# Performance work log

Measured on AMD Instinct MI355X. Metric: run time of the kernel, lower is better.

## Reference

```python
import jax, jax.numpy as jnp
import numpy as np

B, S, DIN, DOUT = 4, 2048, 4096, 4096

def setup_inputs() -> dict:
    key = jax.random.key(0)
    k1, k2, k3, k4 = jax.random.split(key, 4)
    x = jax.random.normal(k1, (B, S, DIN), dtype=jnp.float32)
    # int8-valued weights stored in int32 (harness dtype constraint); values in [-127, 127]
    weight_int8 = jax.random.randint(k2, (DOUT, DIN), -127, 128, dtype=jnp.int32)
    # per-output-channel scales, small positive values typical of int8 quantization
    scale = jax.random.uniform(k3, (DOUT,), dtype=jnp.float32, minval=1e-4, maxval=2e-2)
    bias = jax.random.normal(k4, (DOUT,), dtype=jnp.float32)
    return {"x": x, "weight_int8": weight_int8, "scale": scale, "bias": bias}

def reference(x, weight_int8, scale, bias):
    # Dequantize: w[o, i] = int8[o, i] * scale[o], cast to activation dtype
    w = (weight_int8.astype(jnp.float32) * scale[:, None]).astype(x.dtype)  # [DOUT, DIN]
    # F.linear: y = x @ w.T + bias
    return jnp.einsum('bsi,oi->bso', x, w) + bias
```

## Files before the change

### kernel.cpp

```cpp
#include <hip/hip_runtime.h>
#include <hip/hip_bf16.h>

#define BM 256
#define BN 256
#define BK 64
#define NSLOT 4
#define LDS_BYTES (2 * NSLOT * BM * BK)

typedef float  f32x4  __attribute__((ext_vector_type(4)));
typedef int    i32x4  __attribute__((ext_vector_type(4)));
typedef __bf16 bf16x8 __attribute__((ext_vector_type(8)));
typedef __bf16 bf16x4 __attribute__((ext_vector_type(4)));

__device__ __forceinline__ void gload_lds16(const void* g, void* l) {
    __builtin_amdgcn_global_load_lds(
        (const __attribute__((address_space(1))) void*)g,
        (__attribute__((address_space(3))) void*)l, 16, 0, 0);
}

__global__ __launch_bounds__(256)
void prep_fused(const float* __restrict__ x, const int* __restrict__ w,
                signed char* __restrict__ xq, unsigned* __restrict__ wq,
                float* __restrict__ xs, int K, int M, int n4w, int WB) {
    const int tid = threadIdx.x;
    const int b = blockIdx.x;

    if (b < M) {
        const float* xr = x + (size_t)b * K;
        const int n4 = K / 4;

        float mx = 0.f;
        for (int i = tid; i < n4; i += 256) {
            f32x4 v = ((const f32x4*)xr)[i];
            mx = fmaxf(mx, fmaxf(fmaxf(fabsf(v[0]), fabsf(v[1])),
                                 fmaxf(fabsf(v[2]), fabsf(v[3]))));
        }
#pragma unroll
        for (int off = 32; off; off >>= 1)
            mx = fmaxf(mx, __shfl_xor(mx, off));
        __shared__ float smx[4];
        if ((tid & 63) == 0) smx[tid >> 6] = mx;
        __syncthreads();
        mx = fmaxf(fmaxf(smx[0], smx[1]), fmaxf(smx[2], smx[3]));

        const float inv = mx > 0.f ? 127.f / mx : 0.f;
        if (tid == 0) xs[b] = mx / 127.f;

        unsigned* out = (unsigned*)(xq + (size_t)b * K);
        for (int i = tid; i < n4; i += 256) {
            f32x4 v = ((const f32x4*)xr)[i];
            int q0 = __float2int_rn(v[0] * inv);
            int q1 = __float2int_rn(v[1] * inv);
            int q2 = __float2int_rn(v[2] * inv);
            int q3 = __float2int_rn(v[3] * inv);
            out[i] = (unsigned)(q0 & 255) | ((unsigned)(q1 & 255) << 8) |
                     ((unsigned)(q2 & 255) << 16) | ((unsigned)(q3 & 255) << 24);
        }
    } else {
        int i = (b - M) * 256 + tid;
        const int stride = WB * 256;
        for (; i < n4w; i += stride) {
            i32x4 v = ((const i32x4*)w)[i];
            wq[i] = (unsigned)(v[0] & 255) | ((unsigned)(v[1] & 255) << 8) |
                    ((unsigned)(v[2] & 255) << 16) | ((unsigned)(v[3] & 255) << 24);
        }
    }
}


__global__ __launch_bounds__(512, 2)
void qlin_gemm_i8(const signed char* __restrict__ A,
                  const signed char* __restrict__ B,
                  const float* __restrict__ xs,
                  const float* __restrict__ scale,
                  const float* __restrict__ bias,
                  float* __restrict__ C, int M, int N, int K) {
    extern __shared__ signed char lds[];
    signed char* lA = lds;
    signed char* lB = lds + NSLOT * (BM * BK);

    const int NTN = N / BN;
    const int nwg = gridDim.x;
    int bid = blockIdx.x;
    bid = (bid & 7) * (nwg >> 3) + (bid >> 3);
    const int tm = bid / NTN;
    const int tn = bid % NTN;

    const int tid  = threadIdx.x;
    const int lane = tid & 63;
    const int wid  = tid >> 6;
    const int wr   = wid >> 2;
    const int wc   = wid & 3;

    const int srow0 = wid * 32 + (lane >> 2);
    const int srow1 = srow0 + 16;
    const int gq0 = (lane & 3) ^ ((srow0 >> 1) & 3);
    const int gq1 = (lane & 3) ^ ((srow1 >> 1) & 3);
    const signed char* Ap0 = A + (size_t)(tm * BM + srow0) * K + gq0 * 16;
    const signed char* Ap1 = A + (size_t)(tm * BM + srow1) * K + gq1 * 16;
    const signed char* Bp0 = B + (size_t)(tn * BN + srow0) * K + gq0 * 16;
    const signed char* Bp1 = B + (size_t)(tn * BN + srow1) * K + gq1 * 16;

    const int NT = K / BK;

    auto STAGE_A = [&](int t) {
        signed char* d = lA + (t & (NSLOT - 1)) * (BM * BK) + wid * 2048;
        gload_lds16(Ap0 + t * BK, d);
        gload_lds16(Ap1 + t * BK, d + 1024);
    };
    auto STAGE_B = [&](int t) {
        signed char* d = lB + (t & (NSLOT - 1)) * (BM * BK) + wid * 2048;
        gload_lds16(Bp0 + t * BK, d);
        gload_lds16(Bp1 + t * BK, d + 1024);
    };

    const int fr = lane & 15;
    const int kq = lane >> 4;

    auto AOFF = [&](int mi) {
        const int R = wr * 128 + mi * 16 + fr;
        return R * 64 + ((kq ^ ((R >> 1) & 3)) << 4);
    };
    auto BOFF = [&](int ni) {
        const int R = wc * 64 + ni * 16 + fr;
        return R * 64 + ((kq ^ ((R >> 1) & 3)) << 4);
    };

    i32x4 acc[8][4];
#pragma unroll
    for (int mi = 0; mi < 8; ++mi)
#pragma unroll
        for (int ni = 0; ni < 4; ++ni) {
            acc[mi][ni][0] = 0; acc[mi][ni][1] = 0;
            acc[mi][ni][2] = 0; acc[mi][ni][3] = 0;
        }

    for (int u = 0; u < 3 && u < NT; ++u) { STAGE_A(u); STAGE_B(u); }

    for (int t = 0; t < NT; ++t) {
        const signed char* lAs = lA + (t & (NSLOT - 1)) * (BM * BK);
        const signed char* lBs = lB + (t & (NSLOT - 1)) * (BM * BK);
        const int rem = NT - 1 - t;

        if (rem >= 2)      asm volatile("s_waitcnt vmcnt(8)" ::: "memory");
        else if (rem == 1) asm volatile("s_waitcnt vmcnt(4)" ::: "memory");
        else               asm volatile("s_waitcnt vmcnt(0)" ::: "memory");
        __builtin_amdgcn_s_barrier();

        i32x4 af[8], bf[4];
#pragma unroll
        for (int mi = 0; mi < 8; ++mi)
            af[mi] = *(const i32x4*)(lAs + AOFF(mi));
#pragma unroll
        for (int ni = 0; ni < 4; ++ni)
            bf[ni] = *(const i32x4*)(lBs + BOFF(ni));

        if (t + 3 < NT) { STAGE_A(t + 3); STAGE_B(t + 3); }

#pragma unroll
        for (int mi = 0; mi < 8; ++mi)
#pragma unroll
            for (int ni = 0; ni < 4; ++ni)
                acc[mi][ni] = __builtin_amdgcn_mfma_i32_16x16x64_i8(
                    af[mi], bf[ni], acc[mi][ni], 0, 0, 0);
    }

    const int rb = tm * BM + wr * 128 + (lane >> 4) * 4;
    const int cb = tn * BN + wc * 64 + fr;
#pragma unroll
    for (int mi = 0; mi < 8; ++mi) {
        const int m0 = rb + mi * 16;
        float sm[4];
#pragma unroll
        for (int r = 0; r < 4; ++r) sm[r] = xs[m0 + r];
#pragma unroll
        for (int ni = 0; ni < 4; ++ni) {
            const int n = cb + ni * 16;
            const float sc = scale[n];
            const float bs = bias[n];
#pragma unroll
            for (int r = 0; r < 4; ++r)
                C[(size_t)(m0 + r) * N + n] =
                    fmaf((float)acc[mi][ni][r], sm[r] * sc, bs);
        }
    }
}

#define FBM 128
#define FBK 32

__device__ __forceinline__ int swz_elem(int row, int e) {
    return row * FBK + (e ^ (((row >> 1) & 3) << 3));
}

__global__ __launch_bounds__(256, 2)
void qlin_gemm_reg(const float* __restrict__ A, const int* __restrict__ W,
                   const float* __restrict__ scale, const float* __restrict__ bias,
                   float* __restrict__ C, int M, int N, int K) {
    __shared__ __bf16 lA[2][FBM * FBK];
    __shared__ __bf16 lB[2][FBM * FBK];
    const int NTN = N / FBM;
    const int nwg = gridDim.x;
    int bid = blockIdx.x;
    if ((nwg & 7) == 0) bid = (bid & 7) * (nwg >> 3) + (bid >> 3);
    const int tm = bid / NTN, tn = bid % NTN;
    const int tid = threadIdx.x, lane = tid & 63, wid = tid >> 6;
    const int wr = wid >> 1, wc = wid & 1;
    const int srow0 = tid >> 3, skq = tid & 7;
    const float* aptr = A + (size_t)(tm * FBM + srow0) * K + skq * 4;
    const int*   wptr = W + (size_t)(tn * FBM + srow0) * K + skq * 4;
    const size_t rstride = (size_t)32 * K;
    f32x4 sa[4]; i32x4 sw[4];
    auto LOAD = [&](int t) {
#pragma unroll
        for (int j = 0; j < 4; ++j) {
            sa[j] = *(const f32x4*)(aptr + (size_t)t * FBK + j * rstride);
            sw[j] = *(const i32x4*)(wptr + (size_t)t * FBK + j * rstride);
        }
    };
    auto STORE = [&](int buf) {
#pragma unroll
        for (int j = 0; j < 4; ++j) {
            const int idx = swz_elem(srow0 + j * 32, skq * 4);
            bf16x4 va = { (__bf16)sa[j][0], (__bf16)sa[j][1],
                          (__bf16)sa[j][2], (__bf16)sa[j][3] };
            bf16x4 vw = { (__bf16)(float)sw[j][0], (__bf16)(float)sw[j][1],
                          (__bf16)(float)sw[j][2], (__bf16)(float)sw[j][3] };
            *(bf16x4*)&lA[buf][idx] = va;
            *(bf16x4*)&lB[buf][idx] = vw;
        }
    };
    const f32x4 fzero = {0.f, 0.f, 0.f, 0.f};
    f32x4 acc[4][4];
#pragma unroll
    for (int i = 0; i < 4; ++i)
#pragma unroll
        for (int j = 0; j < 4; ++j) acc[i][j] = fzero;
    const int fr = lane & 15, fks = (lane >> 4) * 8;
    LOAD(0); STORE(0); __syncthreads();
    const int NT = K / FBK;
    for (int t = 0; t < NT; ++t) {
        const int buf = t & 1;
        if (t + 1 < NT) LOAD(t + 1);
        bf16x8 af[4], bfg[4];
#pragma unroll
        for (int mi = 0; mi < 4; ++mi)
            af[mi] = *(const bf16x8*)&lA[buf][swz_elem(wr * 64 + mi * 16 + fr, fks)];
#pragma unroll
        for (int ni = 0; ni < 4; ++ni)
            bfg[ni] = *(const bf16x8*)&lB[buf][swz_elem(wc * 64 + ni * 16 + fr, fks)];
#pragma unroll
        for (int mi = 0; mi < 4; ++mi)
#pragma unroll
            for (int ni = 0; ni < 4; ++ni)
                acc[mi][ni] = __builtin_amdgcn_mfma_f32_16x16x32_bf16(
                    af[mi], bfg[ni], acc[mi][ni], 0, 0, 0);
        if (t + 1 < NT) STORE(buf ^ 1);
        __syncthreads();
    }
    const int row0 = tm * FBM + wr * 64 + (lane >> 4) * 4;
    const int col0 = tn * FBM + wc * 64 + fr;
#pragma unroll
    for (int ni = 0; ni < 4; ++ni) {
        const int n = col0 + ni * 16;
        const float sc = scale[n], bs = bias[n];
#pragma unroll
        for (int mi = 0; mi < 4; ++mi) {
            const int m = row0 + mi * 16;
#pragma unroll
            for (int r = 0; r < 4; ++r)
                C[(size_t)(m + r) * N + n] = fmaf(acc[mi][ni][r], sc, bs);
        }
    }
}

extern "C" void kernel_launch(void* const* d_in, const int* in_sizes, int n_in,
                              void* d_out, int out_size, void* d_ws, size_t ws_size,
                              hipStream_t stream) {
    const float* x     = (const float*)d_in[0];
    const int*   w8    = (const int*)d_in[1];
    const float* scale = (const float*)d_in[2];
    const float* bias  = (const float*)d_in[3];
    float*       out   = (float*)d_out;

    const int DOUT = in_sizes[2];
    const int DIN  = in_sizes[1] / DOUT;
    const int M    = in_sizes[0] / DIN;

    const size_t need = (size_t)M * DIN + (size_t)DOUT * DIN + (size_t)M * 4;
    const int nwg = (M / BM) * (DOUT / BN);
    const bool ok = (ws_size >= need) && (M % BM == 0) && (DOUT % BN == 0) &&
                    (DIN % BK == 0) && (nwg % 8 == 0) && (DIN / BK >= 4) &&
                    (DIN % 4 == 0);
    if (ok) {
        signed char* xq = (signed char*)d_ws;
        signed char* wq = xq + (size_t)M * DIN;
        float*       xs = (float*)(wq + (size_t)DOUT * DIN);
        const int WB = 2048;
        prep_fused<<<M + WB, 256, 0, stream>>>(x, w8, xq, (unsigned*)wq, xs,
                                               DIN, M, DOUT * DIN / 4, WB);
        hipFuncSetAttribute(reinterpret_cast<const void*>(qlin_gemm_i8),
                            hipFuncAttributeMaxDynamicSharedMemorySize, LDS_BYTES);
        qlin_gemm_i8<<<nwg, 512, LDS_BYTES, stream>>>(xq, wq, xs, scale, bias, out,
                                                      M, DOUT, DIN);
    } else {
        dim3 grid((M / FBM) * (DOUT / FBM));
        qlin_gemm_reg<<<grid, 256, 0, stream>>>(x, w8, scale, bias, out, M, DOUT, DIN);
    }
}
```

Before: 188.9 us.

## Load B operand directly into double-buffered registers, bypassing LDS staging

The weight (B) tile is no longer staged through LDS with global_load_lds. Each wave now loads its B fragments straight from global memory into a ping-pong register pair, prefetching one k-tile ahead. A keeps the 4-slot LDS pipeline, so LDS use is halved, which may allow more workgroups per CU and cuts LDS read traffic. In exchange, B is fetched redundantly by the two wave rows and read uncoalesced from global/L2. The wait-count schedule changes to match, and the main loop is unrolled by two, so the number of k-tiles must now be even.

```diff
diff --git a/kernel.cpp b/kernel.cpp
--- a/kernel.cpp
+++ b/kernel.cpp
@@ -5,7 +5,7 @@
 #define BN 256
 #define BK 64
 #define NSLOT 4
-#define LDS_BYTES (2 * NSLOT * BM * BK)
+#define LDS_BYTES (NSLOT * BM * BK)
 
 typedef float  f32x4  __attribute__((ext_vector_type(4)));
 typedef int    i32x4  __attribute__((ext_vector_type(4)));
@@ -77,7 +77,6 @@
                   float* __restrict__ C, int M, int N, int K) {
     extern __shared__ signed char lds[];
     signed char* lA = lds;
-    signed char* lB = lds + NSLOT * (BM * BK);
 
     const int NTN = N / BN;
     const int nwg = gridDim.x;
@@ -98,8 +97,6 @@
     const int gq1 = (lane & 3) ^ ((srow1 >> 1) & 3);
     const signed char* Ap0 = A + (size_t)(tm * BM + srow0) * K + gq0 * 16;
     const signed char* Ap1 = A + (size_t)(tm * BM + srow1) * K + gq1 * 16;
-    const signed char* Bp0 = B + (size_t)(tn * BN + srow0) * K + gq0 * 16;
-    const signed char* Bp1 = B + (size_t)(tn * BN + srow1) * K + gq1 * 16;
 
     const int NT = K / BK;
 
@@ -108,11 +105,6 @@
         gload_lds16(Ap0 + t * BK, d);
         gload_lds16(Ap1 + t * BK, d + 1024);
     };
-    auto STAGE_B = [&](int t) {
-        signed char* d = lB + (t & (NSLOT - 1)) * (BM * BK) + wid * 2048;
-        gload_lds16(Bp0 + t * BK, d);
-        gload_lds16(Bp1 + t * BK, d + 1024);
-    };
 
     const int fr = lane & 15;
     const int kq = lane >> 4;
@@ -121,10 +113,11 @@
         const int R = wr * 128 + mi * 16 + fr;
         return R * 64 + ((kq ^ ((R >> 1) & 3)) << 4);
     };
-    auto BOFF = [&](int ni) {
-        const int R = wc * 64 + ni * 16 + fr;
-        return R * 64 + ((kq ^ ((R >> 1) & 3)) << 4);
-    };
+
+    const signed char* pB[4];
+#pragma unroll
+    for (int ni = 0; ni < 4; ++ni)
+        pB[ni] = B + (size_t)(tn * BN + wc * 64 + ni * 16 + fr) * K + kq * 16;
 
     i32x4 acc[8][4];
 #pragma unroll
@@ -135,34 +128,51 @@
             acc[mi][ni][2] = 0; acc[mi][ni][3] = 0;
         }
 
-    for (int u = 0; u < 3 && u < NT; ++u) { STAGE_A(u); STAGE_B(u); }
-
-    for (int t = 0; t < NT; ++t) {
+    i32x4 bfE[4], bfO[4];
+
+    STAGE_A(0);
+    __builtin_amdgcn_sched_barrier(0);
+#pragma unroll
+    for (int ni = 0; ni < 4; ++ni)
+        bfE[ni] = *(const i32x4*)(pB[ni]);
+    __builtin_amdgcn_sched_barrier(0);
+    if (NT > 1) STAGE_A(1);
+    if (NT > 2) STAGE_A(2);
+
+    auto TILE = [&](int t, i32x4* bcur, i32x4* bnxt) {
         const signed char* lAs = lA + (t & (NSLOT - 1)) * (BM * BK);
-        const signed char* lBs = lB + (t & (NSLOT - 1)) * (BM * BK);
         const int rem = NT - 1 - t;
 
-        if (rem >= 2)      asm volatile("s_waitcnt vmcnt(8)" ::: "memory");
-        else if (rem == 1) asm volatile("s_waitcnt vmcnt(4)" ::: "memory");
+        if (t == 0)        asm volatile("s_waitcnt vmcnt(4)" ::: "memory");
+        else if (rem >= 2) asm volatile("s_waitcnt vmcnt(2)" ::: "memory");
         else               asm volatile("s_waitcnt vmcnt(0)" ::: "memory");
         __builtin_amdgcn_s_barrier();
 
-        i32x4 af[8], bf[4];
+        i32x4 af[8];
 #pragma unroll
         for (int mi = 0; mi < 8; ++mi)
             af[mi] = *(const i32x4*)(lAs + AOFF(mi));
-#pragma unroll
-        for (int ni = 0; ni < 4; ++ni)
-            bf[ni] = *(const i32x4*)(lBs + BOFF(ni));
-
-        if (t + 3 < NT) { STAGE_A(t + 3); STAGE_B(t + 3); }
+
+        if (t + 1 < NT) {
+#pragma unroll
+            for (int ni = 0; ni < 4; ++ni)
+                bnxt[ni] = *(const i32x4*)(pB[ni] + (size_t)(t + 1) * BK);
+        }
+        __builtin_amdgcn_sched_barrier(0);
+        if (t + 3 < NT) STAGE_A(t + 3);
+        __builtin_amdgcn_sched_barrier(0);
 
 #pragma unroll
         for (int mi = 0; mi < 8; ++mi)
 #pragma unroll
             for (int ni = 0; ni < 4; ++ni)
                 acc[mi][ni] = __builtin_amdgcn_mfma_i32_16x16x64_i8(
-                    af[mi], bf[ni], acc[mi][ni], 0, 0, 0);
+                    af[mi], bcur[ni], acc[mi][ni], 0, 0, 0);
+    };
+
+    for (int t = 0; t < NT; t += 2) {
+        TILE(t, bfE, bfO);
+        TILE(t + 1, bfO, bfE);
     }
 
     const int rb = tm * BM + wr * 128 + (lane >> 4) * 4;
@@ -289,9 +299,10 @@
 
     const size_t need = (size_t)M * DIN + (size_t)DOUT * DIN + (size_t)M * 4;
     const int nwg = (M / BM) * (DOUT / BN);
+    const int NT  = DIN / BK;
     const bool ok = (ws_size >= need) && (M % BM == 0) && (DOUT % BN == 0) &&
-                    (DIN % BK == 0) && (nwg % 8 == 0) && (DIN / BK >= 4) &&
-                    (DIN % 4 == 0);
+                    (DIN % BK == 0) && (nwg % 8 == 0) && (NT >= 4) &&
+                    (NT % 2 == 0) && (DIN % 4 == 0);
     if (ok) {
         signed char* xq = (signed char*)d_ws;
         signed char* wq = xq + (size_t)M * DIN;
```

Result: slower. 258.1 us (+36.6%).
